# Performance work log

Hardware: AMD Instinct MI355X
Metric: run time of the kernel (lower is better)

## Reference

```python
import jax, jax.numpy as jnp
import numpy as np

N = 50000
E = 800000
D_IN = 256
D_OUT = 512
GIN_EPS = 0.0      # eps param, train_eps=False -> constant
BN_EPS = 1e-5      # BatchNorm1d default eps


def setup_inputs() -> dict:
    key = jax.random.key(0)
    ks = jax.random.split(key, 9)
    x = jax.random.normal(ks[0], (N, D_IN), dtype=jnp.float32)
    edge_index = jax.random.randint(ks[1], (2, E), 0, N, dtype=jnp.int32)
    edge_weight = jax.random.uniform(ks[2], (E,), dtype=jnp.float32)
    # MLP params: Linear(D_IN,D_OUT) -> BatchNorm1d(D_OUT) -> ReLU -> Linear(D_OUT,D_OUT)
    s1 = 1.0 / np.sqrt(D_IN)
    s2 = 1.0 / np.sqrt(D_OUT)
    W1 = jax.random.uniform(ks[3], (D_IN, D_OUT), jnp.float32, -s1, s1)
    b1 = jax.random.uniform(ks[4], (D_OUT,), jnp.float32, -s1, s1)
    gamma = jnp.ones((D_OUT,), jnp.float32)
    beta = jnp.zeros((D_OUT,), jnp.float32)
    W2 = jax.random.uniform(ks[5], (D_OUT, D_OUT), jnp.float32, -s2, s2)
    b2 = jax.random.uniform(ks[6], (D_OUT,), jnp.float32, -s2, s2)
    return {"x": x, "edge_index": edge_index, "edge_weight": edge_weight,
            "W1": W1, "b1": b1, "gamma": gamma, "beta": beta, "W2": W2, "b2": b2}


def reference(x, edge_index, edge_weight, W1, b1, gamma, beta, W2, b2):
    row, col = edge_index[0], edge_index[1]
    # gather neighbor features, scale by edge weight, scatter-add into destination rows
    msg = edge_weight[:, None] * x[col]                      # (E, D_IN)
    agg = jax.ops.segment_sum(msg, row, num_segments=x.shape[0])  # (N, D_IN)
    h = (1.0 + GIN_EPS) * x + agg                            # GIN combine
    # MLP: Linear -> BatchNorm1d (training-mode batch stats) -> ReLU -> Linear
    h = h @ W1 + b1                                          # (N, D_OUT)
    mean = jnp.mean(h, axis=0)
    var = jnp.var(h, axis=0)                                 # biased, as torch BN uses
    h = (h - mean) * jax.lax.rsqrt(var + BN_EPS) * gamma + beta
    h = jax.nn.relu(h)
    return h @ W2 + b2
```

## Files before the change

kernel.cpp:

```cpp
#include <hip/hip_runtime.h>

#define NNODES 50000
#define NEDGES 800000
#define DIN    256
#define DOUT   512
#define MP     50048
#define BN_EPS 1e-5f
#define NBLK   196

typedef __attribute__((ext_vector_type(8))) __bf16 bf16x8;
typedef __attribute__((ext_vector_type(4))) float  floatx4;

__device__ __forceinline__ ushort f2bf(float f) {
    union { float f; uint u; } v; v.f = f;
    uint u = v.u;
    return (ushort)((u + 0x7FFFu + ((u >> 16) & 1u)) >> 16);
}
__device__ __forceinline__ float bf2f(ushort b) {
    union { uint u; float f; } v; v.u = ((uint)b) << 16;
    return v.f;
}
__device__ __forceinline__ uint bnpack(uint u, float s0, float s1, float h0, float h1) {
    float a = bf2f((ushort)(u & 0xffff)) * s0 + h0;
    float b = bf2f((ushort)(u >> 16))    * s1 + h1;
    a = fmaxf(a, 0.f); b = fmaxf(b, 0.f);
    return (uint)f2bf(a) | ((uint)f2bf(b) << 16);
}

__global__ void k_zero(int* __restrict__ a, float* __restrict__ b) {
    int i = blockIdx.x * 256 + threadIdx.x;
    if (i < 2 * MP) a[i] = 0;
    if (i < 1024)   b[i] = 0.f;
}

__global__ void k_count(const int* __restrict__ ei, int* __restrict__ deg) {
    int e = blockIdx.x * 256 + threadIdx.x;
    atomicAdd(&deg[ei[e]], 1);
}

__global__ void k_scan_block(const int* __restrict__ deg, int* __restrict__ rowstart,
                             int* __restrict__ bsum) {
    __shared__ int s[256];
    int t = threadIdx.x;
    int i = blockIdx.x * 256 + t;
    int v = (i < NNODES) ? deg[i] : 0;
    s[t] = v; __syncthreads();
    #pragma unroll
    for (int d = 1; d < 256; d <<= 1) {
        int add = (t >= d) ? s[t - d] : 0;
        __syncthreads();
        s[t] += add;
        __syncthreads();
    }
    if (i < MP) rowstart[i] = s[t] - v;
    if (t == 255) bsum[blockIdx.x] = s[255];
}

__global__ void k_scan_bsum(const int* __restrict__ bsum, int* __restrict__ bofs) {
    __shared__ int s[256];
    int t = threadIdx.x;
    int v = (t < NBLK) ? bsum[t] : 0;
    s[t] = v; __syncthreads();
    #pragma unroll
    for (int d = 1; d < 256; d <<= 1) {
        int add = (t >= d) ? s[t - d] : 0;
        __syncthreads();
        s[t] += add;
        __syncthreads();
    }
    bofs[t] = s[t] - v;
}

__global__ void k_bucket(const int* __restrict__ ei, const float* __restrict__ ew,
                         const int* __restrict__ rowstart, const int* __restrict__ bofs,
                         int* __restrict__ cursor, int2* __restrict__ cw) {
    int e = blockIdx.x * 256 + threadIdx.x;
    int r = ei[e];
    int c = ei[NEDGES + e];
    float w = ew[e];
    int pos = rowstart[r] + bofs[r >> 8] + atomicAdd(&cursor[r], 1);
    cw[pos] = make_int2(c, __float_as_int(w));
}

__global__ __launch_bounds__(256) void k_aggregate(const float* __restrict__ x,
                                                   const int2* __restrict__ cw,
                                                   const int* __restrict__ rowstart,
                                                   const int* __restrict__ bofs,
                                                   const int* __restrict__ deg,
                                                   ushort* __restrict__ h0b) {
    int t = threadIdx.x;
    int wv = t >> 6, lane = t & 63;
    int n = blockIdx.x * 4 + wv;
    if (n >= MP) return;
    ushort* dst = h0b + (size_t)n * DIN + lane * 4;
    if (n >= NNODES) {
        *(ushort4*)dst = make_ushort4(0, 0, 0, 0);
        return;
    }
    const float* xl = x + lane * 4;
    float4 acc = *(const float4*)(xl + (size_t)n * DIN);
    int start = rowstart[n] + bofs[n >> 8];
    int end   = start + deg[n];
    int j = start;
    for (; j + 3 < end; j += 4) {
        int2 e0 = cw[j], e1 = cw[j + 1], e2 = cw[j + 2], e3 = cw[j + 3];
        float4 v0 = *(const float4*)(xl + (size_t)e0.x * DIN);
        float4 v1 = *(const float4*)(xl + (size_t)e1.x * DIN);
        float4 v2 = *(const float4*)(xl + (size_t)e2.x * DIN);
        float4 v3 = *(const float4*)(xl + (size_t)e3.x * DIN);
        float w0 = __int_as_float(e0.y), w1 = __int_as_float(e1.y);
        float w2 = __int_as_float(e2.y), w3 = __int_as_float(e3.y);
        acc.x += w0 * v0.x; acc.y += w0 * v0.y; acc.z += w0 * v0.z; acc.w += w0 * v0.w;
        acc.x += w1 * v1.x; acc.y += w1 * v1.y; acc.z += w1 * v1.z; acc.w += w1 * v1.w;
        acc.x += w2 * v2.x; acc.y += w2 * v2.y; acc.z += w2 * v2.z; acc.w += w2 * v2.w;
        acc.x += w3 * v3.x; acc.y += w3 * v3.y; acc.z += w3 * v3.z; acc.w += w3 * v3.w;
    }
    for (; j < end; ++j) {
        int2 cv = cw[j];
        float w = __int_as_float(cv.y);
        float4 v = *(const float4*)(xl + (size_t)cv.x * DIN);
        acc.x += w * v.x; acc.y += w * v.y; acc.z += w * v.z; acc.w += w * v.w;
    }
    ushort4 o;
    o.x = f2bf(acc.x); o.y = f2bf(acc.y); o.z = f2bf(acc.z); o.w = f2bf(acc.w);
    *(ushort4*)dst = o;
}

__global__ void k_transpose(const float* __restrict__ W, ushort* __restrict__ WT,
                            int K, int Nc) {
    __shared__ float tile[32][33];
    int t  = threadIdx.x;
    int lx = t & 31, ly = t >> 5;
    int bx = blockIdx.x;
    int by = blockIdx.y;
    #pragma unroll
    for (int p = 0; p < 4; ++p)
        tile[ly + p * 8][lx] = W[(size_t)(by * 32 + ly + p * 8) * Nc + bx * 32 + lx];
    __syncthreads();
    #pragma unroll
    for (int p = 0; p < 4; ++p)
        WT[(size_t)(bx * 32 + ly + p * 8) * K + by * 32 + lx] = f2bf(tile[lx][ly + p * 8]);
}

template<int KDIM, int MODE>
__global__ __launch_bounds__(256) void k_gemm(const ushort* __restrict__ A,
                                              const ushort* __restrict__ BT,
                                              const float* __restrict__ bias,
                                              const float* __restrict__ scale,
                                              const float* __restrict__ shift,
                                              float* __restrict__ gsum,
                                              float* __restrict__ gsq,
                                              void* __restrict__ out) {
    constexpr int LDSK = 64 + 8;
    __shared__ ushort As[128][LDSK];
    __shared__ ushort Bs[128][LDSK];

    int t    = threadIdx.x;
    int bm   = blockIdx.x >> 2;
    int bn   = blockIdx.x & 3;
    int lane = t & 63;
    int w    = t >> 6;
    int wr   = w >> 1, wc = w & 1;
    int l15  = lane & 15, l4 = lane >> 4;

    floatx4 acc[4][4] = {};

    int arow = t >> 3;
    int acol = (t & 7) * 8;
    const size_t abase = (size_t)(bm * 128) * KDIM;
    const size_t bbase = (size_t)(bn * 128) * KDIM;

    for (int k0 = 0; k0 < KDIM; k0 += 64) {
        float4 sc0, sc1, sh0, sh1;
        if (MODE == 2) {
            sc0 = *(const float4*)(scale + k0 + acol);
            sc1 = *(const float4*)(scale + k0 + acol + 4);
            sh0 = *(const float4*)(shift + k0 + acol);
            sh1 = *(const float4*)(shift + k0 + acol + 4);
        }
        #pragma unroll
        for (int p = 0; p < 4; ++p) {
            int row = p * 32 + arow;
            uint4 va = *(const uint4*)(A  + abase + (size_t)row * KDIM + k0 + acol);
            if (MODE == 2) {
                va.x = bnpack(va.x, sc0.x, sc0.y, sh0.x, sh0.y);
                va.y = bnpack(va.y, sc0.z, sc0.w, sh0.z, sh0.w);
                va.z = bnpack(va.z, sc1.x, sc1.y, sh1.x, sh1.y);
                va.w = bnpack(va.w, sc1.z, sc1.w, sh1.z, sh1.w);
            }
            *(uint4*)&As[row][acol] = va;
            uint4 vb = *(const uint4*)(BT + bbase + (size_t)row * KDIM + k0 + acol);
            *(uint4*)&Bs[row][acol] = vb;
        }
        __syncthreads();
        #pragma unroll
        for (int ks = 0; ks < 2; ++ks) {
            bf16x8 af[4], bfr[4];
            #pragma unroll
            for (int m = 0; m < 4; ++m)
                af[m] = *(const bf16x8*)&As[wr * 64 + m * 16 + l15][ks * 32 + l4 * 8];
            #pragma unroll
            for (int n = 0; n < 4; ++n)
                bfr[n] = *(const bf16x8*)&Bs[wc * 64 + n * 16 + l15][ks * 32 + l4 * 8];
            #pragma unroll
            for (int m = 0; m < 4; ++m)
                #pragma unroll
                for (int n = 0; n < 4; ++n)
                    acc[m][n] = __builtin_amdgcn_mfma_f32_16x16x32_bf16(af[m], bfr[n], acc[m][n], 0, 0, 0);
        }
        __syncthreads();
    }

    float csum[4], csq[4];
    #pragma unroll
    for (int n = 0; n < 4; ++n) { csum[n] = 0.f; csq[n] = 0.f; }

    #pragma unroll
    for (int n = 0; n < 4; ++n) {
        int col = bn * 128 + wc * 64 + n * 16 + l15;
        float bv = bias[col];
        #pragma unroll
        for (int m = 0; m < 4; ++m) {
            int rbase = bm * 128 + wr * 64 + m * 16 + l4 * 4;
            #pragma unroll
            for (int i = 0; i < 4; ++i) {
                int grow = rbase + i;
                float vv = acc[m][n][i] + bv;
                if (MODE == 1) {
                    ((ushort*)out)[(size_t)grow * DOUT + col] = f2bf(vv);
                    if (grow < NNODES) { csum[n] += vv; csq[n] += vv * vv; }
                } else {
                    if (grow < NNODES)
                        ((float*)out)[(size_t)grow * DOUT + col] = vv;
                }
            }
        }
    }

    if (MODE == 1) {
        float* sumarr = (float*)&As[0][0];
        float* sqarr  = sumarr + 1024;
        int cid = wr * 4 + l4;
        #pragma unroll
        for (int n = 0; n < 4; ++n) {
            int colL = wc * 64 + n * 16 + l15;
            sumarr[cid * 128 + colL] = csum[n];
            sqarr [cid * 128 + colL] = csq[n];
        }
        __syncthreads();
        if (t < 128) {
            float s = 0.f, q = 0.f;
            #pragma unroll
            for (int k = 0; k < 8; ++k) { s += sumarr[k * 128 + t]; q += sqarr[k * 128 + t]; }
            atomicAdd(&gsum[bn * 128 + t], s);
            atomicAdd(&gsq [bn * 128 + t], q);
        }
    }
}

__global__ void k_bn_finalize(const float* __restrict__ sum, const float* __restrict__ sumsq,
                              const float* __restrict__ gamma, const float* __restrict__ beta,
                              float* __restrict__ scale, float* __restrict__ shift) {
    int c = threadIdx.x;
    float mean = sum[c] * (1.0f / NNODES);
    float var  = sumsq[c] * (1.0f / NNODES) - mean * mean;
    float sc   = gamma[c] * rsqrtf(var + BN_EPS);
    scale[c] = sc;
    shift[c] = beta[c] - mean * sc;
}

extern "C" void kernel_launch(void* const* d_in, const int* in_sizes, int n_in,
                              void* d_out, int out_size, void* d_ws, size_t ws_size,
                              hipStream_t stream) {
    const float* x     = (const float*)d_in[0];
    const int*   ei    = (const int*)  d_in[1];
    const float* ew    = (const float*)d_in[2];
    const float* W1    = (const float*)d_in[3];
    const float* b1    = (const float*)d_in[4];
    const float* gamma = (const float*)d_in[5];
    const float* beta  = (const float*)d_in[6];
    const float* W2    = (const float*)d_in[7];
    const float* b2    = (const float*)d_in[8];

    char* ws = (char*)d_ws;
    ushort* h1b = (ushort*)ws;                       size_t off = (size_t)MP * DOUT * 2;
    ushort* W1T = (ushort*)(ws + off);               off += (size_t)DOUT * DIN * 2;
    ushort* W2T = (ushort*)(ws + off);               off += (size_t)DOUT * DOUT * 2;
    float* colsum   = (float*)(ws + off);            off += 512 * 4;
    float* colsumsq = (float*)(ws + off);            off += 512 * 4;
    float* scale    = (float*)(ws + off);            off += 512 * 4;
    float* shift    = (float*)(ws + off);            off += 512 * 4;

    char* ob = (char*)d_out;
    ushort* h0b     = (ushort*)ob;                   size_t ooff = (size_t)MP * DIN * 2;
    int2*   cw      = (int2*)(ob + ooff);            ooff += (size_t)NEDGES * 8;
    int*    deg     = (int*)(ob + ooff);             ooff += (size_t)MP * 4;
    int*    cursor  = (int*)(ob + ooff);             ooff += (size_t)MP * 4;
    int*    rowstart= (int*)(ob + ooff);             ooff += (size_t)MP * 4;
    int*    bsum    = (int*)(ob + ooff);             ooff += 256 * 4;
    int*    bofs    = (int*)(ob + ooff);             ooff += 256 * 4;
    float*  outp    = (float*)d_out;

    k_zero<<<(2 * MP + 255) / 256, 256, 0, stream>>>(deg, colsum);
    k_transpose<<<dim3(DOUT / 32, DIN / 32),  256, 0, stream>>>(W1, W1T, DIN,  DOUT);
    k_transpose<<<dim3(DOUT / 32, DOUT / 32), 256, 0, stream>>>(W2, W2T, DOUT, DOUT);

    k_count<<<NEDGES / 256, 256, 0, stream>>>(ei, deg);
    k_scan_block<<<NBLK, 256, 0, stream>>>(deg, rowstart, bsum);
    k_scan_bsum<<<1, 256, 0, stream>>>(bsum, bofs);
    k_bucket<<<NEDGES / 256, 256, 0, stream>>>(ei, ew, rowstart, bofs, cursor, cw);

    k_aggregate<<<MP / 4, 256, 0, stream>>>(x, cw, rowstart, bofs, deg, h0b);

    k_gemm<DIN, 1><<<(MP / 128) * 4, 256, 0, stream>>>(h0b, W1T, b1, nullptr, nullptr,
                                                       colsum, colsumsq, (void*)h1b);
    k_bn_finalize<<<1, 512, 0, stream>>>(colsum, colsumsq, gamma, beta, scale, shift);
    k_gemm<DOUT, 2><<<(MP / 128) * 4, 256, 0, stream>>>(h1b, W2T, b2, scale, shift,
                                                        nullptr, nullptr, (void*)outp);
}
```

Baseline: 460.5 us.

## Gather bf16 node features in aggregation and fold prep/BN-finalize kernels

Adds a prep kernel that converts x to bf16 and also does the zeroing and both weight transposes, replacing three launches with one. The aggregation kernel then gathers bf16 rows, which halves the bytes moved by its random neighbor reads. The BN finalize kernel is removed, and the second GEMM recomputes scale and shift per k-slice from the column sums. This trades an extra full pass over x and redundant per-block BN math for less gather traffic and fewer launches. The self term and the neighbor features now lose precision before accumulation.

```diff
diff --git a/kernel.cpp b/kernel.cpp
--- a/kernel.cpp
+++ b/kernel.cpp
@@ -8,6 +8,12 @@
 #define BN_EPS 1e-5f
 #define NBLK   196
 
+#define CVT_B  6250
+#define ZERO_B 391
+#define T1_B   128
+#define T2_B   256
+#define PREP_B (CVT_B + ZERO_B + T1_B + T2_B)
+
 typedef __attribute__((ext_vector_type(8))) __bf16 bf16x8;
 typedef __attribute__((ext_vector_type(4))) float  floatx4;
 
@@ -27,10 +33,44 @@
     return (uint)f2bf(a) | ((uint)f2bf(b) << 16);
 }
 
-__global__ void k_zero(int* __restrict__ a, float* __restrict__ b) {
-    int i = blockIdx.x * 256 + threadIdx.x;
-    if (i < 2 * MP) a[i] = 0;
-    if (i < 1024)   b[i] = 0.f;
+__global__ __launch_bounds__(256) void k_prep(const float* __restrict__ x, ushort* __restrict__ xb,
+                                              const float* __restrict__ W1, ushort* __restrict__ W1T,
+                                              const float* __restrict__ W2, ushort* __restrict__ W2T,
+                                              int* __restrict__ zi, float* __restrict__ zf) {
+    __shared__ float tile[32][33];
+    int b = blockIdx.x;
+    int t = threadIdx.x;
+    if (b < CVT_B) {
+        size_t base = ((size_t)b * 256 + t) * 8;
+        float4 v0 = *(const float4*)(x + base);
+        float4 v1 = *(const float4*)(x + base + 4);
+        uint4 o;
+        o.x = (uint)f2bf(v0.x) | ((uint)f2bf(v0.y) << 16);
+        o.y = (uint)f2bf(v0.z) | ((uint)f2bf(v0.w) << 16);
+        o.z = (uint)f2bf(v1.x) | ((uint)f2bf(v1.y) << 16);
+        o.w = (uint)f2bf(v1.z) | ((uint)f2bf(v1.w) << 16);
+        *(uint4*)(xb + base) = o;
+        return;
+    }
+    b -= CVT_B;
+    if (b < ZERO_B) {
+        int i = b * 256 + t;
+        if (i < 2 * MP) zi[i] = 0;
+        if (i < 1024)   zf[i] = 0.f;
+        return;
+    }
+    b -= ZERO_B;
+    const float* W; ushort* WT; int K, Nc, bx, by;
+    if (b < T1_B) { W = W1; WT = W1T; K = DIN;  Nc = DOUT; bx = b & 15; by = b >> 4; }
+    else { b -= T1_B; W = W2; WT = W2T; K = DOUT; Nc = DOUT; bx = b & 15; by = b >> 4; }
+    int lx = t & 31, ly = t >> 5;
+    #pragma unroll
+    for (int p = 0; p < 4; ++p)
+        tile[ly + p * 8][lx] = W[(size_t)(by * 32 + ly + p * 8) * Nc + bx * 32 + lx];
+    __syncthreads();
+    #pragma unroll
+    for (int p = 0; p < 4; ++p)
+        WT[(size_t)(bx * 32 + ly + p * 8) * K + by * 32 + lx] = f2bf(tile[lx][ly + p * 8]);
 }
 
 __global__ void k_count(const int* __restrict__ ei, int* __restrict__ deg) {
@@ -82,7 +122,7 @@
     cw[pos] = make_int2(c, __float_as_int(w));
 }
 
-__global__ __launch_bounds__(256) void k_aggregate(const float* __restrict__ x,
+__global__ __launch_bounds__(256) void k_aggregate(const ushort* __restrict__ xb,
                                                    const int2* __restrict__ cw,
                                                    const int* __restrict__ rowstart,
                                                    const int* __restrict__ bofs,
@@ -97,57 +137,42 @@
         *(ushort4*)dst = make_ushort4(0, 0, 0, 0);
         return;
     }
-    const float* xl = x + lane * 4;
-    float4 acc = *(const float4*)(xl + (size_t)n * DIN);
+    const ushort* xl = xb + lane * 4;
+    ushort4 sd = *(const ushort4*)(xl + (size_t)n * DIN);
+    float4 acc = make_float4(bf2f(sd.x), bf2f(sd.y), bf2f(sd.z), bf2f(sd.w));
     int start = rowstart[n] + bofs[n >> 8];
     int end   = start + deg[n];
     int j = start;
     for (; j + 3 < end; j += 4) {
         int2 e0 = cw[j], e1 = cw[j + 1], e2 = cw[j + 2], e3 = cw[j + 3];
-        float4 v0 = *(const float4*)(xl + (size_t)e0.x * DIN);
-        float4 v1 = *(const float4*)(xl + (size_t)e1.x * DIN);
-        float4 v2 = *(const float4*)(xl + (size_t)e2.x * DIN);
-        float4 v3 = *(const float4*)(xl + (size_t)e3.x * DIN);
+        ushort4 v0 = *(const ushort4*)(xl + (size_t)e0.x * DIN);
+        ushort4 v1 = *(const ushort4*)(xl + (size_t)e1.x * DIN);
+        ushort4 v2 = *(const ushort4*)(xl + (size_t)e2.x * DIN);
+        ushort4 v3 = *(const ushort4*)(xl + (size_t)e3.x * DIN);
         float w0 = __int_as_float(e0.y), w1 = __int_as_float(e1.y);
         float w2 = __int_as_float(e2.y), w3 = __int_as_float(e3.y);
-        acc.x += w0 * v0.x; acc.y += w0 * v0.y; acc.z += w0 * v0.z; acc.w += w0 * v0.w;
-        acc.x += w1 * v1.x; acc.y += w1 * v1.y; acc.z += w1 * v1.z; acc.w += w1 * v1.w;
-        acc.x += w2 * v2.x; acc.y += w2 * v2.y; acc.z += w2 * v2.z; acc.w += w2 * v2.w;
-        acc.x += w3 * v3.x; acc.y += w3 * v3.y; acc.z += w3 * v3.z; acc.w += w3 * v3.w;
+        acc.x += w0 * bf2f(v0.x); acc.y += w0 * bf2f(v0.y); acc.z += w0 * bf2f(v0.z); acc.w += w0 * bf2f(v0.w);
+        acc.x += w1 * bf2f(v1.x); acc.y += w1 * bf2f(v1.y); acc.z += w1 * bf2f(v1.z); acc.w += w1 * bf2f(v1.w);
+        acc.x += w2 * bf2f(v2.x); acc.y += w2 * bf2f(v2.y); acc.z += w2 * bf2f(v2.z); acc.w += w2 * bf2f(v2.w);
+        acc.x += w3 * bf2f(v3.x); acc.y += w3 * bf2f(v3.y); acc.z += w3 * bf2f(v3.z); acc.w += w3 * bf2f(v3.w);
     }
     for (; j < end; ++j) {
         int2 cv = cw[j];
         float w = __int_as_float(cv.y);
-        float4 v = *(const float4*)(xl + (size_t)cv.x * DIN);
-        acc.x += w * v.x; acc.y += w * v.y; acc.z += w * v.z; acc.w += w * v.w;
+        ushort4 v = *(const ushort4*)(xl + (size_t)cv.x * DIN);
+        acc.x += w * bf2f(v.x); acc.y += w * bf2f(v.y); acc.z += w * bf2f(v.z); acc.w += w * bf2f(v.w);
     }
     ushort4 o;
     o.x = f2bf(acc.x); o.y = f2bf(acc.y); o.z = f2bf(acc.z); o.w = f2bf(acc.w);
     *(ushort4*)dst = o;
-}
-
-__global__ void k_transpose(const float* __restrict__ W, ushort* __restrict__ WT,
-                            int K, int Nc) {
-    __shared__ float tile[32][33];
-    int t  = threadIdx.x;
-    int lx = t & 31, ly = t >> 5;
-    int bx = blockIdx.x;
-    int by = blockIdx.y;
-    #pragma unroll
-    for (int p = 0; p < 4; ++p)
-        tile[ly + p * 8][lx] = W[(size_t)(by * 32 + ly + p * 8) * Nc + bx * 32 + lx];
-    __syncthreads();
-    #pragma unroll
-    for (int p = 0; p < 4; ++p)
-        WT[(size_t)(bx * 32 + ly + p * 8) * K + by * 32 + lx] = f2bf(tile[lx][ly + p * 8]);
 }
 
 template<int KDIM, int MODE>
 __global__ __launch_bounds__(256) void k_gemm(const ushort* __restrict__ A,
                                               const ushort* __restrict__ BT,
                                               const float* __restrict__ bias,
-                                              const float* __restrict__ scale,
-                                              const float* __restrict__ shift,
+                                              const float* __restrict__ gamma,
+                                              const float* __restrict__ beta,
                                               float* __restrict__ gsum,
                                               float* __restrict__ gsq,
                                               void* __restrict__ out) {
@@ -171,22 +196,27 @@
     const size_t bbase = (size_t)(bn * 128) * KDIM;
 
     for (int k0 = 0; k0 < KDIM; k0 += 64) {
-        float4 sc0, sc1, sh0, sh1;
+        float scl[8], shf[8];
         if (MODE == 2) {
-            sc0 = *(const float4*)(scale + k0 + acol);
-            sc1 = *(const float4*)(scale + k0 + acol + 4);
-            sh0 = *(const float4*)(shift + k0 + acol);
-            sh1 = *(const float4*)(shift + k0 + acol + 4);
+            #pragma unroll
+            for (int jj = 0; jj < 8; ++jj) {
+                int c = k0 + acol + jj;
+                float mean = gsum[c] * (1.0f / NNODES);
+                float var  = gsq[c]  * (1.0f / NNODES) - mean * mean;
+                float s    = gamma[c] * rsqrtf(var + BN_EPS);
+                scl[jj] = s;
+                shf[jj] = beta[c] - mean * s;
+            }
         }
         #pragma unroll
         for (int p = 0; p < 4; ++p) {
             int row = p * 32 + arow;
             uint4 va = *(const uint4*)(A  + abase + (size_t)row * KDIM + k0 + acol);
             if (MODE == 2) {
-                va.x = bnpack(va.x, sc0.x, sc0.y, sh0.x, sh0.y);
-                va.y = bnpack(va.y, sc0.z, sc0.w, sh0.z, sh0.w);
-                va.z = bnpack(va.z, sc1.x, sc1.y, sh1.x, sh1.y);
-                va.w = bnpack(va.w, sc1.z, sc1.w, sh1.z, sh1.w);
+                va.x = bnpack(va.x, scl[0], scl[1], shf[0], shf[1]);
+                va.y = bnpack(va.y, scl[2], scl[3], shf[2], shf[3]);
+                va.z = bnpack(va.z, scl[4], scl[5], shf[4], shf[5]);
+                va.w = bnpack(va.w, scl[6], scl[7], shf[6], shf[7]);
             }
             *(uint4*)&As[row][acol] = va;
             uint4 vb = *(const uint4*)(BT + bbase + (size_t)row * KDIM + k0 + acol);
@@ -256,17 +286,6 @@
             atomicAdd(&gsq [bn * 128 + t], q);
         }
     }
-}
-
-__global__ void k_bn_finalize(const float* __restrict__ sum, const float* __restrict__ sumsq,
-                              const float* __restrict__ gamma, const float* __restrict__ beta,
-                              float* __restrict__ scale, float* __restrict__ shift) {
-    int c = threadIdx.x;
-    float mean = sum[c] * (1.0f / NNODES);
-    float var  = sumsq[c] * (1.0f / NNODES) - mean * mean;
-    float sc   = gamma[c] * rsqrtf(var + BN_EPS);
-    scale[c] = sc;
-    shift[c] = beta[c] - mean * sc;
 }
 
 extern "C" void kernel_launch(void* const* d_in, const int* in_sizes, int n_in,
@@ -288,11 +307,10 @@
     ushort* W2T = (ushort*)(ws + off);               off += (size_t)DOUT * DOUT * 2;
     float* colsum   = (float*)(ws + off);            off += 512 * 4;
     float* colsumsq = (float*)(ws + off);            off += 512 * 4;
-    float* scale    = (float*)(ws + off);            off += 512 * 4;
-    float* shift    = (float*)(ws + off);            off += 512 * 4;
 
     char* ob = (char*)d_out;
     ushort* h0b     = (ushort*)ob;                   size_t ooff = (size_t)MP * DIN * 2;
+    ushort* xb      = (ushort*)(ob + ooff);          ooff += (size_t)NNODES * DIN * 2;
     int2*   cw      = (int2*)(ob + ooff);            ooff += (size_t)NEDGES * 8;
     int*    deg     = (int*)(ob + ooff);             ooff += (size_t)MP * 4;
     int*    cursor  = (int*)(ob + ooff);             ooff += (size_t)MP * 4;
@@ -301,20 +319,17 @@
     int*    bofs    = (int*)(ob + ooff);             ooff += 256 * 4;
     float*  outp    = (float*)d_out;
 
-    k_zero<<<(2 * MP + 255) / 256, 256, 0, stream>>>(deg, colsum);
-    k_transpose<<<dim3(DOUT / 32, DIN / 32),  256, 0, stream>>>(W1, W1T, DIN,  DOUT);
-    k_transpose<<<dim3(DOUT / 32, DOUT / 32), 256, 0, stream>>>(W2, W2T, DOUT, DOUT);
+    k_prep<<<PREP_B, 256, 0, stream>>>(x, xb, W1, W1T, W2, W2T, deg, colsum);
 
     k_count<<<NEDGES / 256, 256, 0, stream>>>(ei, deg);
     k_scan_block<<<NBLK, 256, 0, stream>>>(deg, rowstart, bsum);
     k_scan_bsum<<<1, 256, 0, stream>>>(bsum, bofs);
     k_bucket<<<NEDGES / 256, 256, 0, stream>>>(ei, ew, rowstart, bofs, cursor, cw);
 
-    k_aggregate<<<MP / 4, 256, 0, stream>>>(x, cw, rowstart, bofs, deg, h0b);
+    k_aggregate<<<MP / 4, 256, 0, stream>>>(xb, cw, rowstart, bofs, deg, h0b);
 
     k_gemm<DIN, 1><<<(MP / 128) * 4, 256, 0, stream>>>(h0b, W1T, b1, nullptr, nullptr,
                                                        colsum, colsumsq, (void*)h1b);
-    k_bn_finalize<<<1, 512, 0, stream>>>(colsum, colsumsq, gamma, beta, scale, shift);
-    k_gemm<DOUT, 2><<<(MP / 128) * 4, 256, 0, stream>>>(h1b, W2T, b2, scale, shift,
-                                                        nullptr, nullptr, (void*)outp);
-}
+    k_gemm<DOUT, 2><<<(MP / 128) * 4, 256, 0, stream>>>(h1b, W2T, b2, gamma, beta,
+                                                        colsum, colsumsq, (void*)outp);
+}
```

Measured after the change: 438.1 us. 4.9% less time.
